# Optimization experiments

Hardware: AMD Instinct MI355X
Metric: run time of the kernel (lower is better)

Reference implementation:

```python
import jax, jax.numpy as jnp
import numpy as np

N, E = 50000, 600000
D_IN, D_H, D_OUT = 128, 128, 128


def sage_conv(x, src, dst, w_l, b_l, w_r, num_nodes):
    """PyG SAGEConv with mean aggregation: lin_l(mean_j x_j) + lin_r(x_i).
    lin_l has bias, lin_r has no bias (PyG defaults)."""
    msgs = x[src]                                                    # [E, d] gather
    agg = jax.ops.segment_sum(msgs, dst, num_segments=num_nodes)    # [N, d] scatter-add
    deg = jax.ops.segment_sum(jnp.ones((src.shape[0],), x.dtype), dst,
                              num_segments=num_nodes)               # [N]
    agg = agg / jnp.maximum(deg, 1.0)[:, None]                      # mean
    return agg @ w_l + b_l + x @ w_r


def setup_inputs() -> dict:
    key = jax.random.key(0)
    ks = jax.random.split(key, 7)
    s = 1.0 / np.sqrt(D_IN)
    return {
        "x": jax.random.normal(ks[0], (N, D_IN), dtype=jnp.float32),
        "edge_index": jax.random.randint(ks[1], (2, E), 0, N, dtype=jnp.int64),
        "w_l1": jax.random.normal(ks[2], (D_IN, D_H), dtype=jnp.float32) * s,
        "b_l1": jnp.zeros((D_H,), dtype=jnp.float32),
        "w_r1": jax.random.normal(ks[3], (D_IN, D_H), dtype=jnp.float32) * s,
        "w_l2": jax.random.normal(ks[4], (D_H, D_OUT), dtype=jnp.float32) * s,
        "b_l2": jnp.zeros((D_OUT,), dtype=jnp.float32),
        "w_r2": jax.random.normal(ks[5], (D_H, D_OUT), dtype=jnp.float32) * s,
    }


def reference(x, edge_index, w_l1, b_l1, w_r1, w_l2, b_l2, w_r2):
    src, dst = edge_index[0], edge_index[1]
    num_nodes = x.shape[0]
    h = sage_conv(x, src, dst, w_l1, b_l1, w_r1, num_nodes)
    h = jax.nn.relu(h)
    # F.dropout with training=False is the identity (inference reference)
    out = sage_conv(h, src, dst, w_l2, b_l2, w_r2, num_nodes)
    return out
```

## Files before the change

kernel.cpp:

```cpp
#include <hip/hip_runtime.h>
#include <hip/hip_bf16.h>


#define D 128
#define PAD 64

typedef __attribute__((ext_vector_type(8))) short bf16x8;
typedef __attribute__((ext_vector_type(4))) float f32x4;

__device__ __forceinline__ unsigned short f2bf(float f) {
    __hip_bfloat16 b = __float2bfloat16(f);
    return *(unsigned short*)&b;
}
__device__ __forceinline__ float bf_lo(unsigned u) { return __uint_as_float(u << 16); }
__device__ __forceinline__ float bf_hi(unsigned u) { return __uint_as_float(u & 0xffff0000u); }

__global__ __launch_bounds__(256) void prep_kernel(
    const float* __restrict__ x, unsigned short* __restrict__ xb, int n4,
    const float* __restrict__ w0, const float* __restrict__ w1,
    const float* __restrict__ w2, const float* __restrict__ w3,
    unsigned short* __restrict__ o0, unsigned short* __restrict__ o1,
    unsigned short* __restrict__ o2, unsigned short* __restrict__ o3,
    int* __restrict__ cursor, int n, int nb_f2bf) {
    int b = blockIdx.x;
    int tid = threadIdx.x;
    if (b < nb_f2bf) {
        int i = b * 256 + tid;
        if (i < n4) {
            float4 v = ((const float4*)x)[i];
            ushort4 o;
            o.x = f2bf(v.x); o.y = f2bf(v.y); o.z = f2bf(v.z); o.w = f2bf(v.w);
            ((ushort4*)xb)[i] = o;
        }
    } else if (b < nb_f2bf + 256) {
        int t = (b - nb_f2bf) * 256 + tid;
        int m = t >> 14;
        int r = t & 16383;
        int f = r >> 9;
        int q = r & 511;
        int lane = q >> 3, j = q & 7;
        int kt = f & 3, c = f >> 2;
        int k  = kt * 32 + (lane >> 4) * 8 + j;
        int nn = c * 16 + (lane & 15);
        const float* w = (m == 0) ? w0 : (m == 1) ? w1 : (m == 2) ? w2 : w3;
        unsigned short* o = (m == 0) ? o0 : (m == 1) ? o1 : (m == 2) ? o2 : o3;
        o[r] = f2bf(w[k * 128 + nn]);
    } else {
        int i = (b - nb_f2bf - 256) * 256 + tid;
        if (i < n) cursor[i] = 0;
    }
}

__global__ void fill_pad_kernel(const int* __restrict__ src, const int* __restrict__ dst,
                                int* __restrict__ cursor, unsigned short* __restrict__ csr,
                                int E) {
    int i = blockIdx.x * blockDim.x + threadIdx.x;
    int e0 = i * 2;
    if (e0 < E) {
        int2 s2 = ((const int2*)src)[i];
        int2 d2 = ((const int2*)dst)[i];
        int p = atomicAdd(&cursor[d2.x], 1);
        if (p < PAD) csr[d2.x * PAD + p] = (unsigned short)s2.x;
        if (e0 + 1 < E) {
            p = atomicAdd(&cursor[d2.y], 1);
            if (p < PAD) csr[d2.y * PAD + p] = (unsigned short)s2.y;
        }
    }
}

__global__ __launch_bounds__(256) void aggregate_bf16_kernel(
    const unsigned short* __restrict__ feat, const int* __restrict__ deg,
    const unsigned short* __restrict__ csr, unsigned short* __restrict__ agg, int n) {
    int pair = (blockIdx.x * 256 + threadIdx.x) >> 6;
    int lane = threadIdx.x & 63;
    int m0 = pair * 2;
    if (m0 >= n) return;
    int m1 = m0 + 1;
    const int g  = lane >> 4;
    const int s  = lane & 15;
    const int gg = g & 1;

    int cnt0 = deg[m0]; if (cnt0 > PAD) cnt0 = PAD;
    int cnt1 = (m1 < n) ? deg[m1] : 0; if (cnt1 > PAD) cnt1 = PAD;
    const int mycnt = (g < 2) ? cnt0 : cnt1;
    const int mybeg = ((g < 2) ? m0 : m1) * PAD;
    int cmax = cnt0 > cnt1 ? cnt0 : cnt1;

    float a0 = 0.f, a1 = 0.f, a2 = 0.f, a3 = 0.f;
    float a4 = 0.f, a5 = 0.f, a6 = 0.f, a7 = 0.f;

    for (int j = 0; j < cmax; j += 8) {
        uint4 u[4];
        float w[4];
#pragma unroll
        for (int k = 0; k < 4; ++k) {
            int p = j + 2 * k + gg;
            w[k] = (p < mycnt) ? 1.0f : 0.0f;
            int pc = (p < mycnt) ? p : 0;
            int idx = csr[mybeg + pc];
            u[k] = *(const uint4*)(feat + (size_t)idx * D + s * 8);
        }
#pragma unroll
        for (int k = 0; k < 4; ++k) {
            a0 += w[k] * bf_lo(u[k].x); a1 += w[k] * bf_hi(u[k].x);
            a2 += w[k] * bf_lo(u[k].y); a3 += w[k] * bf_hi(u[k].y);
            a4 += w[k] * bf_lo(u[k].z); a5 += w[k] * bf_hi(u[k].z);
            a6 += w[k] * bf_lo(u[k].w); a7 += w[k] * bf_hi(u[k].w);
        }
    }

    a0 += __shfl_xor(a0, 16, 64);
    a1 += __shfl_xor(a1, 16, 64);
    a2 += __shfl_xor(a2, 16, 64);
    a3 += __shfl_xor(a3, 16, 64);
    a4 += __shfl_xor(a4, 16, 64);
    a5 += __shfl_xor(a5, 16, 64);
    a6 += __shfl_xor(a6, 16, 64);
    a7 += __shfl_xor(a7, 16, 64);

    if (gg == 0) {
        int mym = (g < 2) ? m0 : m1;
        if (mym < n) {
            int c = mycnt;
            float sc = 1.0f / (float)(c > 0 ? c : 1);
            uint4 o;
            o.x = ((unsigned)f2bf(a1 * sc) << 16) | (unsigned)f2bf(a0 * sc);
            o.y = ((unsigned)f2bf(a3 * sc) << 16) | (unsigned)f2bf(a2 * sc);
            o.z = ((unsigned)f2bf(a5 * sc) << 16) | (unsigned)f2bf(a4 * sc);
            o.w = ((unsigned)f2bf(a7 * sc) << 16) | (unsigned)f2bf(a6 * sc);
            *(uint4*)(agg + (size_t)mym * D + s * 8) = o;
        }
    }
}

__global__ __launch_bounds__(256) void gemm_mfma_kernel(
    const unsigned short* __restrict__ A, const unsigned short* __restrict__ X,
    const unsigned short* __restrict__ WfL, const unsigned short* __restrict__ WfR,
    const float* __restrict__ bias, unsigned short* __restrict__ out_bf,
    float* __restrict__ out_f32, int n, int mode, int ntiles) {
    __shared__ unsigned short lds[2][32][512];

    const int tid = threadIdx.x;
    {
        const uint4* srcL = (const uint4*)WfL;
        const uint4* srcR = (const uint4*)WfR;
        uint4* dst = (uint4*)&lds[0][0][0];
#pragma unroll
        for (int it = 0; it < 8; ++it) {
            int i = it * 256 + tid;
            dst[i]        = srcL[i];
            dst[2048 + i] = srcR[i];
        }
    }
    __syncthreads();

    const int wid = tid >> 6;
    const int lane = tid & 63;
    const int quad = lane >> 4;
    const int l16 = lane & 15;

    for (int tile = blockIdx.x; tile < ntiles; tile += gridDim.x) {
        const int row0 = tile * 64 + wid * 16;
        int m = row0 + l16;
        if (m >= n) m = n - 1;

        bf16x8 af[2][4];
        const unsigned short* apA = A + (size_t)m * D + quad * 8;
        const unsigned short* apX = X + (size_t)m * D + quad * 8;
#pragma unroll
        for (int kt = 0; kt < 4; ++kt) {
            af[0][kt] = *(const bf16x8*)(apA + kt * 32);
            af[1][kt] = *(const bf16x8*)(apX + kt * 32);
        }

        f32x4 acc[8];
#pragma unroll
        for (int c = 0; c < 8; ++c) acc[c] = (f32x4){0.f, 0.f, 0.f, 0.f};

#pragma unroll
        for (int half = 0; half < 2; ++half) {
#pragma unroll
            for (int kt = 0; kt < 4; ++kt) {
#pragma unroll
                for (int c = 0; c < 8; ++c) {
                    bf16x8 bfrag = *(const bf16x8*)&lds[half][c * 4 + kt][lane * 8];
                    acc[c] = __builtin_amdgcn_mfma_f32_16x16x32_bf16(af[half][kt], bfrag, acc[c], 0, 0, 0);
                }
            }
        }

#pragma unroll
        for (int c = 0; c < 8; ++c) {
            int col = c * 16 + l16;
            float bb = bias[col];
#pragma unroll
            for (int r = 0; r < 4; ++r) {
                int row = row0 + quad * 4 + r;
                if (row < n) {
                    float v = acc[c][r] + bb;
                    if (mode) {
                        v = fmaxf(v, 0.0f);
                        out_bf[(size_t)row * D + col] = f2bf(v);
                    } else {
                        out_f32[(size_t)row * D + col] = v;
                    }
                }
            }
        }
    }
}


extern "C" void kernel_launch(void* const* d_in, const int* in_sizes, int n_in,
                              void* d_out, int out_size, void* d_ws, size_t ws_size,
                              hipStream_t stream) {
    const float* x   = (const float*)d_in[0];
    const int*   edg = (const int*)d_in[1];
    const float* wl1 = (const float*)d_in[2];
    const float* bl1 = (const float*)d_in[3];
    const float* wr1 = (const float*)d_in[4];
    const float* wl2 = (const float*)d_in[5];
    const float* bl2 = (const float*)d_in[6];
    const float* wr2 = (const float*)d_in[7];
    float* out = (float*)d_out;

    const int N = in_sizes[0] / D;
    const int E = in_sizes[1] / 2;
    const int* src = edg;
    const int* dst = edg + E;
    const int NB = (N + 255) / 256;

    char* ws = (char*)d_ws;
    size_t off = 0;
    auto carve = [&](size_t bytes) -> char* {
        char* p = ws + off;
        off = (off + bytes + 255) & ~(size_t)255;
        return p;
    };
    int*   cursor  = (int*)  carve((size_t)N * 4);
    unsigned short* csr = (unsigned short*)carve((size_t)N * PAD * 2);
    unsigned short* xb   = (unsigned short*)carve((size_t)N * D * 2);
    unsigned short* hb   = (unsigned short*)carve((size_t)N * D * 2);
    unsigned short* aggb = (unsigned short*)carve((size_t)N * D * 2);
    unsigned short* wtl1 = (unsigned short*)carve(16384 * 2);
    unsigned short* wtr1 = (unsigned short*)carve(16384 * 2);
    unsigned short* wtl2 = (unsigned short*)carve(16384 * 2);
    unsigned short* wtr2 = (unsigned short*)carve(16384 * 2);
    (void)ws_size;

    int n4 = N * D / 4;
    int nb_f2bf = (n4 + 255) / 256;
    int prep_blocks = nb_f2bf + 256 + NB;

    prep_kernel<<<prep_blocks, 256, 0, stream>>>(
        x, xb, n4, wl1, wr1, wl2, wr2, wtl1, wtr1, wtl2, wtr2, cursor, N, nb_f2bf);

    int epairs = (E + 1) / 2;
    int eb = (epairs + 255) / 256;
    fill_pad_kernel<<<eb, 256, 0, stream>>>(src, dst, cursor, csr, E);

    int pairs = (N + 1) / 2;
    int agg_blocks = (pairs + 3) / 4;
    int ntiles = (N + 63) / 64;
    int gemm_blocks = (ntiles + 1) / 2;

    aggregate_bf16_kernel<<<agg_blocks, 256, 0, stream>>>(xb, cursor, csr, aggb, N);
    gemm_mfma_kernel<<<gemm_blocks, 256, 0, stream>>>(aggb, xb, wtl1, wtr1, bl1, hb, (float*)nullptr, N, 1, ntiles);

    aggregate_bf16_kernel<<<agg_blocks, 256, 0, stream>>>(hb, cursor, csr, aggb, N);
    gemm_mfma_kernel<<<gemm_blocks, 256, 0, stream>>>(aggb, hb, wtl2, wtr2, bl2, (unsigned short*)nullptr, out, N, 0, ntiles);
}
```

Baseline: 208.6 us.

## Fuse neighbor aggregation into the MFMA GEMM through an LDS tile

Merges the mean-aggregation kernel and the dual-weight MFMA GEMM into one kernel per layer. Each 64-row block gathers neighbour features, writes the bf16 mean into a swizzled LDS tile, then feeds it directly to MFMA. This removes the global round trip of the aggregated matrix and two launches. Weight fragments are now read from global/L2 instead of being staged in LDS, and each block handles one tile rather than looping persistently, which adds per-block weight traffic and can leave more load imbalance across blocks.

```diff
diff --git a/kernel.cpp b/kernel.cpp
--- a/kernel.cpp
+++ b/kernel.cpp
@@ -68,142 +68,128 @@
     }
 }
 
-__global__ __launch_bounds__(256) void aggregate_bf16_kernel(
-    const unsigned short* __restrict__ feat, const int* __restrict__ deg,
-    const unsigned short* __restrict__ csr, unsigned short* __restrict__ agg, int n) {
-    int pair = (blockIdx.x * 256 + threadIdx.x) >> 6;
-    int lane = threadIdx.x & 63;
-    int m0 = pair * 2;
-    if (m0 >= n) return;
-    int m1 = m0 + 1;
-    const int g  = lane >> 4;
-    const int s  = lane & 15;
-    const int gg = g & 1;
-
-    int cnt0 = deg[m0]; if (cnt0 > PAD) cnt0 = PAD;
-    int cnt1 = (m1 < n) ? deg[m1] : 0; if (cnt1 > PAD) cnt1 = PAD;
-    const int mycnt = (g < 2) ? cnt0 : cnt1;
-    const int mybeg = ((g < 2) ? m0 : m1) * PAD;
-    int cmax = cnt0 > cnt1 ? cnt0 : cnt1;
-
-    float a0 = 0.f, a1 = 0.f, a2 = 0.f, a3 = 0.f;
-    float a4 = 0.f, a5 = 0.f, a6 = 0.f, a7 = 0.f;
-
-    for (int j = 0; j < cmax; j += 8) {
-        uint4 u[4];
-        float w[4];
-#pragma unroll
-        for (int k = 0; k < 4; ++k) {
-            int p = j + 2 * k + gg;
-            w[k] = (p < mycnt) ? 1.0f : 0.0f;
-            int pc = (p < mycnt) ? p : 0;
-            int idx = csr[mybeg + pc];
-            u[k] = *(const uint4*)(feat + (size_t)idx * D + s * 8);
-        }
-#pragma unroll
-        for (int k = 0; k < 4; ++k) {
-            a0 += w[k] * bf_lo(u[k].x); a1 += w[k] * bf_hi(u[k].x);
-            a2 += w[k] * bf_lo(u[k].y); a3 += w[k] * bf_hi(u[k].y);
-            a4 += w[k] * bf_lo(u[k].z); a5 += w[k] * bf_hi(u[k].z);
-            a6 += w[k] * bf_lo(u[k].w); a7 += w[k] * bf_hi(u[k].w);
-        }
-    }
-
-    a0 += __shfl_xor(a0, 16, 64);
-    a1 += __shfl_xor(a1, 16, 64);
-    a2 += __shfl_xor(a2, 16, 64);
-    a3 += __shfl_xor(a3, 16, 64);
-    a4 += __shfl_xor(a4, 16, 64);
-    a5 += __shfl_xor(a5, 16, 64);
-    a6 += __shfl_xor(a6, 16, 64);
-    a7 += __shfl_xor(a7, 16, 64);
-
-    if (gg == 0) {
-        int mym = (g < 2) ? m0 : m1;
-        if (mym < n) {
-            int c = mycnt;
-            float sc = 1.0f / (float)(c > 0 ? c : 1);
-            uint4 o;
-            o.x = ((unsigned)f2bf(a1 * sc) << 16) | (unsigned)f2bf(a0 * sc);
-            o.y = ((unsigned)f2bf(a3 * sc) << 16) | (unsigned)f2bf(a2 * sc);
-            o.z = ((unsigned)f2bf(a5 * sc) << 16) | (unsigned)f2bf(a4 * sc);
-            o.w = ((unsigned)f2bf(a7 * sc) << 16) | (unsigned)f2bf(a6 * sc);
-            *(uint4*)(agg + (size_t)mym * D + s * 8) = o;
-        }
-    }
-}
-
-__global__ __launch_bounds__(256) void gemm_mfma_kernel(
-    const unsigned short* __restrict__ A, const unsigned short* __restrict__ X,
+__global__ __launch_bounds__(256, 4) void fused_agg_gemm_kernel(
+    const unsigned short* __restrict__ feat,
     const unsigned short* __restrict__ WfL, const unsigned short* __restrict__ WfR,
+    const int* __restrict__ deg, const unsigned short* __restrict__ csr,
     const float* __restrict__ bias, unsigned short* __restrict__ out_bf,
-    float* __restrict__ out_f32, int n, int mode, int ntiles) {
-    __shared__ unsigned short lds[2][32][512];
-
-    const int tid = threadIdx.x;
+    float* __restrict__ out_f32, int n, int mode) {
+    __shared__ unsigned short ldsa[64][128];
+
+    const int tid  = threadIdx.x;
+    const int wid  = tid >> 6;
+    const int lane = tid & 63;
+    const int row0 = blockIdx.x * 64;
+
     {
-        const uint4* srcL = (const uint4*)WfL;
-        const uint4* srcR = (const uint4*)WfR;
-        uint4* dst = (uint4*)&lds[0][0][0];
-#pragma unroll
-        for (int it = 0; it < 8; ++it) {
-            int i = it * 256 + tid;
-            dst[i]        = srcL[i];
-            dst[2048 + i] = srcR[i];
+        const int g  = lane >> 4;
+        const int s  = lane & 15;
+        const int gg = g & 1;
+        const int nsel = g >> 1;
+
+        for (int ii = 0; ii < 8; ++ii) {
+            int r0 = wid * 16 + ii * 2;
+            int m0 = row0 + r0;
+            int m1 = m0 + 1;
+            int cnt0 = (m0 < n) ? deg[m0] : 0; if (cnt0 > PAD) cnt0 = PAD;
+            int cnt1 = (m1 < n) ? deg[m1] : 0; if (cnt1 > PAD) cnt1 = PAD;
+            int mym   = nsel ? m1 : m0;
+            int mycnt = nsel ? cnt1 : cnt0;
+            int mybeg = (mym < n ? mym : 0) * PAD;
+            int cmax  = cnt0 > cnt1 ? cnt0 : cnt1;
+
+            float a0 = 0.f, a1 = 0.f, a2 = 0.f, a3 = 0.f;
+            float a4 = 0.f, a5 = 0.f, a6 = 0.f, a7 = 0.f;
+
+            for (int j = 0; j < cmax; j += 8) {
+                uint4 u[4];
+                float w[4];
+#pragma unroll
+                for (int k = 0; k < 4; ++k) {
+                    int p = j + 2 * k + gg;
+                    w[k] = (p < mycnt) ? 1.0f : 0.0f;
+                    int pc = (p < mycnt) ? p : 0;
+                    int idx = csr[mybeg + pc];
+                    u[k] = *(const uint4*)(feat + (size_t)idx * D + s * 8);
+                }
+#pragma unroll
+                for (int k = 0; k < 4; ++k) {
+                    a0 += w[k] * bf_lo(u[k].x); a1 += w[k] * bf_hi(u[k].x);
+                    a2 += w[k] * bf_lo(u[k].y); a3 += w[k] * bf_hi(u[k].y);
+                    a4 += w[k] * bf_lo(u[k].z); a5 += w[k] * bf_hi(u[k].z);
+                    a6 += w[k] * bf_lo(u[k].w); a7 += w[k] * bf_hi(u[k].w);
+                }
+            }
+
+            a0 += __shfl_xor(a0, 16, 64);
+            a1 += __shfl_xor(a1, 16, 64);
+            a2 += __shfl_xor(a2, 16, 64);
+            a3 += __shfl_xor(a3, 16, 64);
+            a4 += __shfl_xor(a4, 16, 64);
+            a5 += __shfl_xor(a5, 16, 64);
+            a6 += __shfl_xor(a6, 16, 64);
+            a7 += __shfl_xor(a7, 16, 64);
+
+            if (gg == 0) {
+                int r = r0 + nsel;
+                float sc = 1.0f / (float)(mycnt > 0 ? mycnt : 1);
+                uint4 o;
+                o.x = ((unsigned)f2bf(a1 * sc) << 16) | (unsigned)f2bf(a0 * sc);
+                o.y = ((unsigned)f2bf(a3 * sc) << 16) | (unsigned)f2bf(a2 * sc);
+                o.z = ((unsigned)f2bf(a5 * sc) << 16) | (unsigned)f2bf(a4 * sc);
+                o.w = ((unsigned)f2bf(a7 * sc) << 16) | (unsigned)f2bf(a6 * sc);
+                *(uint4*)&ldsa[r][(s ^ (r & 15)) * 8] = o;
+            }
         }
     }
     __syncthreads();
 
-    const int wid = tid >> 6;
-    const int lane = tid & 63;
     const int quad = lane >> 4;
-    const int l16 = lane & 15;
-
-    for (int tile = blockIdx.x; tile < ntiles; tile += gridDim.x) {
-        const int row0 = tile * 64 + wid * 16;
-        int m = row0 + l16;
-        if (m >= n) m = n - 1;
-
-        bf16x8 af[2][4];
-        const unsigned short* apA = A + (size_t)m * D + quad * 8;
-        const unsigned short* apX = X + (size_t)m * D + quad * 8;
+    const int l16  = lane & 15;
+    const int rloc = wid * 16 + l16;
+    int mc = row0 + rloc;
+    if (mc >= n) mc = n - 1;
+
+    bf16x8 af[2][4];
+    const unsigned short* apX = feat + (size_t)mc * D + quad * 8;
+#pragma unroll
+    for (int kt = 0; kt < 4; ++kt) {
+        int c = kt * 4 + quad;
+        af[0][kt] = *(const bf16x8*)&ldsa[rloc][(c ^ (rloc & 15)) * 8];
+        af[1][kt] = *(const bf16x8*)(apX + kt * 32);
+    }
+
+    f32x4 acc[8];
+#pragma unroll
+    for (int c = 0; c < 8; ++c) acc[c] = (f32x4){0.f, 0.f, 0.f, 0.f};
+
+#pragma unroll
+    for (int half = 0; half < 2; ++half) {
+        const unsigned short* wp = half ? WfR : WfL;
 #pragma unroll
         for (int kt = 0; kt < 4; ++kt) {
-            af[0][kt] = *(const bf16x8*)(apA + kt * 32);
-            af[1][kt] = *(const bf16x8*)(apX + kt * 32);
-        }
-
-        f32x4 acc[8];
-#pragma unroll
-        for (int c = 0; c < 8; ++c) acc[c] = (f32x4){0.f, 0.f, 0.f, 0.f};
-
-#pragma unroll
-        for (int half = 0; half < 2; ++half) {
-#pragma unroll
-            for (int kt = 0; kt < 4; ++kt) {
-#pragma unroll
-                for (int c = 0; c < 8; ++c) {
-                    bf16x8 bfrag = *(const bf16x8*)&lds[half][c * 4 + kt][lane * 8];
-                    acc[c] = __builtin_amdgcn_mfma_f32_16x16x32_bf16(af[half][kt], bfrag, acc[c], 0, 0, 0);
-                }
-            }
-        }
-
-#pragma unroll
-        for (int c = 0; c < 8; ++c) {
-            int col = c * 16 + l16;
-            float bb = bias[col];
-#pragma unroll
-            for (int r = 0; r < 4; ++r) {
-                int row = row0 + quad * 4 + r;
-                if (row < n) {
-                    float v = acc[c][r] + bb;
-                    if (mode) {
-                        v = fmaxf(v, 0.0f);
-                        out_bf[(size_t)row * D + col] = f2bf(v);
-                    } else {
-                        out_f32[(size_t)row * D + col] = v;
-                    }
+#pragma unroll
+            for (int c = 0; c < 8; ++c) {
+                bf16x8 bfrag = *(const bf16x8*)(wp + (size_t)(c * 4 + kt) * 512 + lane * 8);
+                acc[c] = __builtin_amdgcn_mfma_f32_16x16x32_bf16(af[half][kt], bfrag, acc[c], 0, 0, 0);
+            }
+        }
+    }
+
+#pragma unroll
+    for (int c = 0; c < 8; ++c) {
+        int col = c * 16 + l16;
+        float bb = bias[col];
+#pragma unroll
+        for (int r = 0; r < 4; ++r) {
+            int row = row0 + wid * 16 + quad * 4 + r;
+            if (row < n) {
+                float v = acc[c][r] + bb;
+                if (mode) {
+                    v = fmaxf(v, 0.0f);
+                    out_bf[(size_t)row * D + col] = f2bf(v);
+                } else {
+                    out_f32[(size_t)row * D + col] = v;
                 }
             }
         }
@@ -241,7 +227,6 @@
     unsigned short* csr = (unsigned short*)carve((size_t)N * PAD * 2);
     unsigned short* xb   = (unsigned short*)carve((size_t)N * D * 2);
     unsigned short* hb   = (unsigned short*)carve((size_t)N * D * 2);
-    unsigned short* aggb = (unsigned short*)carve((size_t)N * D * 2);
     unsigned short* wtl1 = (unsigned short*)carve(16384 * 2);
     unsigned short* wtr1 = (unsigned short*)carve(16384 * 2);
     unsigned short* wtl2 = (unsigned short*)carve(16384 * 2);
@@ -259,14 +244,11 @@
     int eb = (epairs + 255) / 256;
     fill_pad_kernel<<<eb, 256, 0, stream>>>(src, dst, cursor, csr, E);
 
-    int pairs = (N + 1) / 2;
-    int agg_blocks = (pairs + 3) / 4;
     int ntiles = (N + 63) / 64;
-    int gemm_blocks = (ntiles + 1) / 2;
-
-    aggregate_bf16_kernel<<<agg_blocks, 256, 0, stream>>>(xb, cursor, csr, aggb, N);
-    gemm_mfma_kernel<<<gemm_blocks, 256, 0, stream>>>(aggb, xb, wtl1, wtr1, bl1, hb, (float*)nullptr, N, 1, ntiles);
-
-    aggregate_bf16_kernel<<<agg_blocks, 256, 0, stream>>>(hb, cursor, csr, aggb, N);
-    gemm_mfma_kernel<<<gemm_blocks, 256, 0, stream>>>(aggb, hb, wtl2, wtr2, bl2, (unsigned short*)nullptr, out, N, 0, ntiles);
-}
+
+    fused_agg_gemm_kernel<<<ntiles, 256, 0, stream>>>(
+        xb, wtl1, wtr1, cursor, csr, bl1, hb, (float*)nullptr, N, 1);
+
+    fused_agg_gemm_kernel<<<ntiles, 256, 0, stream>>>(
+        hb, wtl2, wtr2, cursor, csr, bl2, (unsigned short*)nullptr, out, N, 0);
+}
```

Result: faster. 201.0 us (-3.6%).
